# Kernel optimization log

Hardware: AMD Instinct MI355X
Metric: run time of the kernel (lower is better)

## Reference

```python
import jax, jax.numpy as jnp
import numpy as np

VOCAB, EMBED, HIDDEN, LAYERS = 128, 512, 1024, 2
BATCH, SEQ = 64, 512


def _lstm_layer(x, w_ih, w_hh, b_ih, b_hh):
    # x: [B, T, In]; w_ih: [4H, In]; w_hh: [4H, H]
    B, T, _ = x.shape
    H = w_hh.shape[1]
    # Precompute the input contribution for all timesteps at once: [B, T, 4H]
    xin = jnp.einsum('bti,gi->btg', x, w_ih) + b_ih + b_hh

    def step(carry, xt):
        h, c = carry
        z = xt + h @ w_hh.T                      # [B, 4H]
        i, f, g, o = jnp.split(z, 4, axis=-1)    # PyTorch gate order i,f,g,o
        i = jax.nn.sigmoid(i)
        f = jax.nn.sigmoid(f)
        g = jnp.tanh(g)
        o = jax.nn.sigmoid(o)
        c = f * c + i * g
        h = o * jnp.tanh(c)
        return (h, c), h

    h0 = jnp.zeros((B, H), x.dtype)
    c0 = jnp.zeros((B, H), x.dtype)
    _, hs = jax.lax.scan(step, (h0, c0), jnp.swapaxes(xin, 0, 1))  # [T, B, H]
    return jnp.swapaxes(hs, 0, 1)                                   # [B, T, H]


def setup_inputs() -> dict:
    key = jax.random.key(0)
    ks = jax.random.split(key, 12)
    s_e = 1.0 / np.sqrt(EMBED)
    s_h = 1.0 / np.sqrt(HIDDEN)
    return {
        'x': jax.random.randint(ks[0], (BATCH, SEQ), 0, VOCAB, dtype=jnp.int32),
        'embedding': jax.random.normal(ks[1], (VOCAB, EMBED), jnp.float32),
        'w_ih_0': jax.random.normal(ks[2], (4 * HIDDEN, EMBED), jnp.float32) * s_e,
        'w_hh_0': jax.random.normal(ks[3], (4 * HIDDEN, HIDDEN), jnp.float32) * s_h,
        'b_ih_0': jax.random.normal(ks[4], (4 * HIDDEN,), jnp.float32) * s_h,
        'b_hh_0': jax.random.normal(ks[5], (4 * HIDDEN,), jnp.float32) * s_h,
        'w_ih_1': jax.random.normal(ks[6], (4 * HIDDEN, HIDDEN), jnp.float32) * s_h,
        'w_hh_1': jax.random.normal(ks[7], (4 * HIDDEN, HIDDEN), jnp.float32) * s_h,
        'b_ih_1': jax.random.normal(ks[8], (4 * HIDDEN,), jnp.float32) * s_h,
        'b_hh_1': jax.random.normal(ks[9], (4 * HIDDEN,), jnp.float32) * s_h,
        'fc_w': jax.random.normal(ks[10], (VOCAB, HIDDEN), jnp.float32) * s_h,
        'fc_b': jax.random.normal(ks[11], (VOCAB,), jnp.float32) * s_h,
    }


def reference(x, embedding, w_ih_0, w_hh_0, b_ih_0, b_hh_0,
              w_ih_1, w_hh_1, b_ih_1, b_hh_1, fc_w, fc_b):
    emb = embedding[x]                                   # [B, T, E]
    h1 = _lstm_layer(emb, w_ih_0, w_hh_0, b_ih_0, b_hh_0)  # [B, T, H]
    h2 = _lstm_layer(h1, w_ih_1, w_hh_1, b_ih_1, b_hh_1)   # [B, T, H]
    return h2 @ fc_w.T + fc_b                            # [B, T, V]
```

## Files before the change

### kernel.cpp

```cpp
#include <hip/hip_runtime.h>


typedef _Float16 v8h __attribute__((ext_vector_type(8)));
typedef float v4f __attribute__((ext_vector_type(4)));
typedef _Float16 h2v __attribute__((ext_vector_type(2)));
typedef unsigned long long u64t;

__device__ __forceinline__ float sigf(float x) {
  return 1.0f / (1.0f + __expf(-x));
}
__device__ __forceinline__ float tanhfast(float x) {
  return 1.0f - 2.0f / (1.0f + __expf(2.0f * x));
}

__global__ __launch_bounds__(256) void prep_kernel(
    const float* __restrict__ emb, const float* __restrict__ w_ih0,
    const float* __restrict__ b_ih0, const float* __restrict__ b_hh0,
    const float* __restrict__ fc_w, _Float16* __restrict__ tableV,
    _Float16* __restrict__ fcwT, unsigned* __restrict__ zbuf,
    unsigned* __restrict__ bar) {
  const int blk = blockIdx.x, tid = threadIdx.x;
  if (blk < 2048) {
    const int C = blk * 2 + (tid >> 7);
    const int v = tid & 127;
    const int row =
        ((C >> 2) & 3) * 1024 + (C >> 5) * 8 + ((C >> 4) & 1) * 4 + (C & 3);
    float acc = b_ih0[row] + b_hh0[row];
    const float* er = emb + v * 512;
    const float* wr = w_ih0 + row * 512;
#pragma unroll 4
    for (int k = 0; k < 512; ++k) acc = fmaf(er[k], wr[k], acc);
    tableV[v * 4096 + C] = (_Float16)acc;
  } else if (blk < 2560) {
    const int idx = (blk - 2048) * 256 + tid;
    const int v = idx & 127, k = idx >> 7;
    fcwT[k * 128 + v] = (_Float16)fc_w[v * 1024 + k];
  } else if (blk < 2592) {
    const int idx = (blk - 2560) * 256 + tid;
#pragma unroll
    for (int q = 0; q < 16; ++q) zbuf[idx * 16 + q] = 0u;
  } else {
    for (int i = tid; i < 512; i += 256) bar[i] = 0u;
  }
}

__global__ __launch_bounds__(768, 1) void lstm_mfma(
    const int* __restrict__ x, const _Float16* __restrict__ tableV,
    const float* __restrict__ w_hh0, const float* __restrict__ w_ih1,
    const float* __restrict__ w_hh1, const float* __restrict__ b_ih1,
    const float* __restrict__ b_hh1, _Float16* __restrict__ hseq,
    unsigned* __restrict__ bar) {
  __shared__ __align__(16) float zs[12 * 4 * 8 * 32];

  const int tid = threadIdx.x, blk = blockIdx.x;
  const int w = tid >> 6, l = tid & 63;
  const int lane16 = l & 15, quad = l >> 4;
  const int xcd = blk & 7, bidx = blk >> 3;
  const int m = bidx >> 4, cg = xcd * 16 + (bidx & 15);
  const int kc = (w < 4) ? w : (w - 4);

  v8h breg0[8], breg1[8];
  {
    const int g = lane16 >> 2, j = lane16 & 3;
    const float* Wsrc;
    int kbase;
    if (w < 4) {
      Wsrc = w_hh0;
      kbase = kc * 256;
    } else {
      const int kcomb = kc * 256;
      if (kcomb < 1024) {
        Wsrc = w_ih1;
        kbase = kcomb;
      } else {
        Wsrc = w_hh1;
        kbase = kcomb - 1024;
      }
    }
#pragma unroll
    for (int cb = 0; cb < 2; ++cb) {
      const int row = g * 1024 + cg * 8 + cb * 4 + j;
      const float* rp = Wsrc + row * 1024 + kbase + quad * 8;
#pragma unroll
      for (int kk = 0; kk < 8; ++kk) {
        const float4 f0 = *(const float4*)(rp + kk * 32);
        const float4 f1 = *(const float4*)(rp + kk * 32 + 4);
        v8h b;
        b[0] = (_Float16)f0.x; b[1] = (_Float16)f0.y;
        b[2] = (_Float16)f0.z; b[3] = (_Float16)f0.w;
        b[4] = (_Float16)f1.x; b[5] = (_Float16)f1.y;
        b[6] = (_Float16)f1.z; b[7] = (_Float16)f1.w;
        if (cb == 0) breg0[kk] = b; else breg1[kk] = b;
      }
    }
  }

  const int oj = l & 7, ojj = l & 3, ocb = (l >> 2) & 1;
  const int ob = (w & 3) * 8 + (l >> 3);
  const int obg = m * 32 + ob;
  const int colp = (lane16 & 3) * 4 + (lane16 >> 2);
  const int cswz = colp ^ ((quad & 1) << 4);
  const int rr = ob & 3, rqo = ob >> 2;
  const int rcol = (ocb * 16 + ojj * 4) ^ ((rqo & 1) << 4);

  v4f bias4 = {0.f, 0.f, 0.f, 0.f};
  if (w >= 4 && w < 8) {
#pragma unroll
    for (int g = 0; g < 4; ++g) {
      const int row = g * 1024 + cg * 8 + ocb * 4 + ojj;
      bias4[g] = b_ih1[row] + b_hh1[row];
    }
  }
  _Float16 tvh[4] = {0, 0, 0, 0};
  if (w < 4) {
    const int xv = x[obg * 512];
#pragma unroll
    for (int g = 0; g < 4; ++g)
      tvh[g] = tableV[xv * 4096 + cg * 32 + ocb * 16 + g * 4 + ojj];
  }

  float cst = 0.0f;
  const int gq = blk & 7;

  for (int it = 0; it <= 512; ++it) {
    const _Float16* hr = hseq + (size_t)it * 131072;
    _Float16* hw = hseq + (size_t)(it + 1) * 131072;

    v4f a00 = {0, 0, 0, 0}, a01 = {0, 0, 0, 0};
    v4f a10 = {0, 0, 0, 0}, a11 = {0, 0, 0, 0};
    const bool active = (w < 4) ? (it < 512) : (it >= 1);
    if (active) {
      const _Float16* a0p = hr + (m * 32 + lane16) * 2048 + kc * 256 + quad * 8;
      const _Float16* a1p = a0p + 16 * 2048;
      v8h A0[8], A1[8];
#pragma unroll
      for (int kk = 0; kk < 8; ++kk) A0[kk] = *(const v8h*)(a0p + kk * 32);
#pragma unroll
      for (int kk = 0; kk < 8; ++kk) A1[kk] = *(const v8h*)(a1p + kk * 32);
      __builtin_amdgcn_sched_barrier(0);
#pragma unroll
      for (int kk = 0; kk < 8; ++kk) {
        a00 = __builtin_amdgcn_mfma_f32_16x16x32_f16(A0[kk], breg0[kk], a00, 0, 0, 0);
        a10 = __builtin_amdgcn_mfma_f32_16x16x32_f16(A0[kk], breg1[kk], a10, 0, 0, 0);
      }
#pragma unroll
      for (int kk = 0; kk < 8; ++kk) {
        a01 = __builtin_amdgcn_mfma_f32_16x16x32_f16(A1[kk], breg0[kk], a01, 0, 0, 0);
        a11 = __builtin_amdgcn_mfma_f32_16x16x32_f16(A1[kk], breg1[kk], a11, 0, 0, 0);
      }
    }

#pragma unroll
    for (int r = 0; r < 4; ++r) {
      float* zp = &zs[((w * 4 + r) * 8 + quad) * 32];
      zp[cswz] = a00[r];
      zp[128 + cswz] = a01[r];
      zp[cswz ^ 16] = a10[r];
      zp[128 + (cswz ^ 16)] = a11[r];
    }
    __syncthreads();

    const bool do0 = (w < 4) && (it < 512);
    const bool do1 = (w >= 4 && w < 8) && (it >= 1);
    if (do0 || do1) {
      v4f z;
      if (do0) {
        z[0] = (float)tvh[0]; z[1] = (float)tvh[1];
        z[2] = (float)tvh[2]; z[3] = (float)tvh[3];
#pragma unroll
        for (int wv = 0; wv < 4; ++wv)
          z += *(const v4f*)&zs[((wv * 4 + rr) * 8 + rqo) * 32 + rcol];
      } else {
        z = bias4;
#pragma unroll
        for (int wv = 4; wv < 12; ++wv)
          z += *(const v4f*)&zs[((wv * 4 + rr) * 8 + rqo) * 32 + rcol];
      }
      const float ig = sigf(z[0]), fg = sigf(z[1]);
      const float gg = tanhfast(z[2]), og = sigf(z[3]);
      cst = fg * cst + ig * gg;
      const float hv = og * tanhfast(cst);

      const unsigned hu =
          (unsigned)__builtin_bit_cast(unsigned short, (_Float16)hv);
      const unsigned p1 = (unsigned)__shfl_xor((int)hu, 1, 64);
      const unsigned lo = (oj & 1) ? ((p1 & 0xffffu) | (hu << 16))
                                   : ((hu & 0xffffu) | (p1 << 16));
      const unsigned p2 = (unsigned)__shfl_xor((int)lo, 2, 64);
      if ((oj & 3) == 0) {
        const u64t val = (u64t)lo | ((u64t)p2 << 32);
        if (do0) {
          __hip_atomic_store((u64t*)(hw + obg * 2048 + cg * 8 + oj), val,
                             __ATOMIC_RELAXED, __HIP_MEMORY_SCOPE_AGENT);
        } else {
          __hip_atomic_store((u64t*)(hw + obg * 2048 + 1024 + cg * 8 + oj),
                             val, __ATOMIC_RELAXED, __HIP_MEMORY_SCOPE_AGENT);
        }
      }
    }

    if (w < 4 && it + 1 < 512) {
      const int xv = x[obg * 512 + it + 1];
#pragma unroll
      for (int g = 0; g < 4; ++g)
        tvh[g] = tableV[xv * 4096 + cg * 32 + ocb * 16 + g * 4 + ojj];
    }

    if (it < 512) {
      asm volatile("s_waitcnt vmcnt(0)" ::: "memory");
      __syncthreads();
      if (tid == 0) {
        atomicAdd(&bar[(m * 8 + gq) * 16], 1u);
        const unsigned tgt = 16u * (unsigned)(it + 1);
        for (;;) {
          unsigned v[8];
#pragma unroll
          for (int g = 0; g < 8; ++g)
            v[g] = __hip_atomic_load(&bar[(m * 8 + g) * 16], __ATOMIC_RELAXED,
                                     __HIP_MEMORY_SCOPE_AGENT);
          unsigned mn = v[0];
#pragma unroll
          for (int g = 1; g < 8; ++g) mn = (v[g] < mn) ? v[g] : mn;
          if (mn >= tgt) break;
          __builtin_amdgcn_s_sleep(1);
        }
      }
      __syncthreads();
      asm volatile("" ::: "memory");
    }
  }
}

__global__ __launch_bounds__(256, 2) void fc_kernel(
    const _Float16* __restrict__ hseq, const _Float16* __restrict__ fcwT,
    const float* __restrict__ fc_b, float* __restrict__ out) {
  __shared__ float hl[16][1024];
  const int tid = threadIdx.x;
  const int t = blockIdx.x >> 2, bs = blockIdx.x & 3;
  const int v = tid & 127, hh = tid >> 7;

  const h2v* hp = (const h2v*)hseq;
  const size_t base = (size_t)(t + 2) * 65536 + 512;
  for (int idx = tid; idx < 8192; idx += 256) {
    const int bl = idx >> 9, kp = idx & 511;
    const h2v pr = hp[base + (size_t)((bs * 16 + bl)) * 1024 + kp];
    hl[bl][2 * kp] = (float)pr.x;
    hl[bl][2 * kp + 1] = (float)pr.y;
  }
  __syncthreads();

  float acc[8];
#pragma unroll
  for (int i = 0; i < 8; ++i) acc[i] = 0.0f;
  const int bl0 = hh * 8;
#pragma unroll 1
  for (int k4 = 0; k4 < 256; ++k4) {
    const int k = k4 * 4;
    const float w0 = (float)fcwT[(k + 0) * 128 + v];
    const float w1 = (float)fcwT[(k + 1) * 128 + v];
    const float w2 = (float)fcwT[(k + 2) * 128 + v];
    const float w3 = (float)fcwT[(k + 3) * 128 + v];
#pragma unroll
    for (int i = 0; i < 8; ++i) {
      const float4 hv = *(const float4*)&hl[bl0 + i][k];
      acc[i] += hv.x * w0 + hv.y * w1 + hv.z * w2 + hv.w * w3;
    }
  }
  const float bias = fc_b[v];
#pragma unroll
  for (int i = 0; i < 8; ++i) {
    const int bb = bs * 16 + bl0 + i;
    out[(bb * 512 + t) * 128 + v] = acc[i] + bias;
  }
}

extern "C" void kernel_launch(void* const* d_in, const int* in_sizes, int n_in,
                              void* d_out, int out_size, void* d_ws,
                              size_t ws_size, hipStream_t stream) {
  const int* x = (const int*)d_in[0];
  const float* emb = (const float*)d_in[1];
  const float* w_ih0 = (const float*)d_in[2];
  const float* w_hh0 = (const float*)d_in[3];
  const float* b_ih0 = (const float*)d_in[4];
  const float* b_hh0 = (const float*)d_in[5];
  const float* w_ih1 = (const float*)d_in[6];
  const float* w_hh1 = (const float*)d_in[7];
  const float* b_ih1 = (const float*)d_in[8];
  const float* b_hh1 = (const float*)d_in[9];
  const float* fc_w = (const float*)d_in[10];
  const float* fc_b = (const float*)d_in[11];
  float* out = (float*)d_out;

  char* ws = (char*)d_ws;
  _Float16* tableV = (_Float16*)(ws);
  _Float16* fcwT = (_Float16*)(ws + 1048576);
  unsigned* bar = (unsigned*)(ws + 1310720);
  _Float16* hseq = (_Float16*)(ws + 1376256);
  unsigned* zb = (unsigned*)(ws + 1376256);

  prep_kernel<<<2593, 256, 0, stream>>>(emb, w_ih0, b_ih0, b_hh0, fc_w,
                                        tableV, fcwT, zb, bar);

  const _Float16* tableVc = tableV;
  _Float16* hseqa = hseq;
  unsigned* bara = bar;
  void* args[] = {(void*)&x,     (void*)&tableVc, (void*)&w_hh0,
                  (void*)&w_ih1, (void*)&w_hh1,   (void*)&b_ih1,
                  (void*)&b_hh1, (void*)&hseqa,   (void*)&bara};
  hipLaunchCooperativeKernel(lstm_mfma, dim3(256), dim3(768), args, 0, stream);

  fc_kernel<<<2048, 256, 0, stream>>>(hseq, fcwT, fc_b, out);
}
```

Measured before the change: 4.878 ms.

## Reuse layer-0 h tile for both w_hh0 and w_ih1 products, shrink block to 8 waves

Warps 0-3 now hold both the w_hh0 and w_ih1 weight slices in registers and apply both to the same loaded h1 tile, so the layer-1 input projection no longer needs separate waves that reload the same h data. The block shrinks from 12 to 8 waves, and launch bounds change to 512 threads with 2 blocks per CU. This removes redundant global loads of h and frees waves, but it doubles the B-register footprint in waves 0-3, which increases register pressure and risks spills. It also puts more serial MFMA work on those waves.

```diff
diff --git a/kernel.cpp b/kernel.cpp
--- a/kernel.cpp
+++ b/kernel.cpp
@@ -44,7 +44,7 @@
   }
 }
 
-__global__ __launch_bounds__(768, 1) void lstm_mfma(
+__global__ __launch_bounds__(512, 2) void lstm_mfma(
     const int* __restrict__ x, const _Float16* __restrict__ tableV,
     const float* __restrict__ w_hh0, const float* __restrict__ w_ih1,
     const float* __restrict__ w_hh1, const float* __restrict__ b_ih1,
@@ -57,26 +57,12 @@
   const int lane16 = l & 15, quad = l >> 4;
   const int xcd = blk & 7, bidx = blk >> 3;
   const int m = bidx >> 4, cg = xcd * 16 + (bidx & 15);
-  const int kc = (w < 4) ? w : (w - 4);
-
-  v8h breg0[8], breg1[8];
+
+  v8h bh0[8], bh1[8], bi0[8], bi1[8];
   {
     const int g = lane16 >> 2, j = lane16 & 3;
-    const float* Wsrc;
-    int kbase;
-    if (w < 4) {
-      Wsrc = w_hh0;
-      kbase = kc * 256;
-    } else {
-      const int kcomb = kc * 256;
-      if (kcomb < 1024) {
-        Wsrc = w_ih1;
-        kbase = kcomb;
-      } else {
-        Wsrc = w_hh1;
-        kbase = kcomb - 1024;
-      }
-    }
+    const float* Wsrc = (w < 4) ? w_hh0 : w_hh1;
+    const int kbase = (w < 4) ? w * 256 : w * 256 - 1024;
 #pragma unroll
     for (int cb = 0; cb < 2; ++cb) {
       const int row = g * 1024 + cg * 8 + cb * 4 + j;
@@ -90,7 +76,25 @@
         b[2] = (_Float16)f0.z; b[3] = (_Float16)f0.w;
         b[4] = (_Float16)f1.x; b[5] = (_Float16)f1.y;
         b[6] = (_Float16)f1.z; b[7] = (_Float16)f1.w;
-        if (cb == 0) breg0[kk] = b; else breg1[kk] = b;
+        if (cb == 0) bh0[kk] = b; else bh1[kk] = b;
+      }
+    }
+    if (w < 4) {
+#pragma unroll
+      for (int cb = 0; cb < 2; ++cb) {
+        const int row = g * 1024 + cg * 8 + cb * 4 + j;
+        const float* rp = w_ih1 + row * 1024 + w * 256 + quad * 8;
+#pragma unroll
+        for (int kk = 0; kk < 8; ++kk) {
+          const float4 f0 = *(const float4*)(rp + kk * 32);
+          const float4 f1 = *(const float4*)(rp + kk * 32 + 4);
+          v8h b;
+          b[0] = (_Float16)f0.x; b[1] = (_Float16)f0.y;
+          b[2] = (_Float16)f0.z; b[3] = (_Float16)f0.w;
+          b[4] = (_Float16)f1.x; b[5] = (_Float16)f1.y;
+          b[6] = (_Float16)f1.z; b[7] = (_Float16)f1.w;
+          if (cb == 0) bi0[kk] = b; else bi1[kk] = b;
+        }
       }
     }
   }
@@ -104,7 +108,7 @@
   const int rcol = (ocb * 16 + ojj * 4) ^ ((rqo & 1) << 4);
 
   v4f bias4 = {0.f, 0.f, 0.f, 0.f};
-  if (w >= 4 && w < 8) {
+  if (w >= 4) {
 #pragma unroll
     for (int g = 0; g < 4; ++g) {
       const int row = g * 1024 + cg * 8 + ocb * 4 + ojj;
@@ -126,11 +130,13 @@
     const _Float16* hr = hseq + (size_t)it * 131072;
     _Float16* hw = hseq + (size_t)(it + 1) * 131072;
 
-    v4f a00 = {0, 0, 0, 0}, a01 = {0, 0, 0, 0};
-    v4f a10 = {0, 0, 0, 0}, a11 = {0, 0, 0, 0};
-    const bool active = (w < 4) ? (it < 512) : (it >= 1);
-    if (active) {
-      const _Float16* a0p = hr + (m * 32 + lane16) * 2048 + kc * 256 + quad * 8;
+    v4f p00 = {0, 0, 0, 0}, p01 = {0, 0, 0, 0};
+    v4f p10 = {0, 0, 0, 0}, p11 = {0, 0, 0, 0};
+    v4f q00 = {0, 0, 0, 0}, q01 = {0, 0, 0, 0};
+    v4f q10 = {0, 0, 0, 0}, q11 = {0, 0, 0, 0};
+    const bool ld = (w < 4) || (it >= 1);
+    if (ld) {
+      const _Float16* a0p = hr + (m * 32 + lane16) * 2048 + w * 256 + quad * 8;
       const _Float16* a1p = a0p + 16 * 2048;
       v8h A0[8], A1[8];
 #pragma unroll
@@ -138,30 +144,64 @@
 #pragma unroll
       for (int kk = 0; kk < 8; ++kk) A1[kk] = *(const v8h*)(a1p + kk * 32);
       __builtin_amdgcn_sched_barrier(0);
-#pragma unroll
-      for (int kk = 0; kk < 8; ++kk) {
-        a00 = __builtin_amdgcn_mfma_f32_16x16x32_f16(A0[kk], breg0[kk], a00, 0, 0, 0);
-        a10 = __builtin_amdgcn_mfma_f32_16x16x32_f16(A0[kk], breg1[kk], a10, 0, 0, 0);
-      }
-#pragma unroll
-      for (int kk = 0; kk < 8; ++kk) {
-        a01 = __builtin_amdgcn_mfma_f32_16x16x32_f16(A1[kk], breg0[kk], a01, 0, 0, 0);
-        a11 = __builtin_amdgcn_mfma_f32_16x16x32_f16(A1[kk], breg1[kk], a11, 0, 0, 0);
-      }
-    }
-
-#pragma unroll
-    for (int r = 0; r < 4; ++r) {
-      float* zp = &zs[((w * 4 + r) * 8 + quad) * 32];
-      zp[cswz] = a00[r];
-      zp[128 + cswz] = a01[r];
-      zp[cswz ^ 16] = a10[r];
-      zp[128 + (cswz ^ 16)] = a11[r];
+      if (w < 4) {
+        if (it < 512) {
+#pragma unroll
+          for (int kk = 0; kk < 8; ++kk) {
+            p00 = __builtin_amdgcn_mfma_f32_16x16x32_f16(A0[kk], bh0[kk], p00, 0, 0, 0);
+            p10 = __builtin_amdgcn_mfma_f32_16x16x32_f16(A0[kk], bh1[kk], p10, 0, 0, 0);
+            p01 = __builtin_amdgcn_mfma_f32_16x16x32_f16(A1[kk], bh0[kk], p01, 0, 0, 0);
+            p11 = __builtin_amdgcn_mfma_f32_16x16x32_f16(A1[kk], bh1[kk], p11, 0, 0, 0);
+          }
+        }
+        if (it >= 1) {
+#pragma unroll
+          for (int kk = 0; kk < 8; ++kk) {
+            q00 = __builtin_amdgcn_mfma_f32_16x16x32_f16(A0[kk], bi0[kk], q00, 0, 0, 0);
+            q10 = __builtin_amdgcn_mfma_f32_16x16x32_f16(A0[kk], bi1[kk], q10, 0, 0, 0);
+            q01 = __builtin_amdgcn_mfma_f32_16x16x32_f16(A1[kk], bi0[kk], q01, 0, 0, 0);
+            q11 = __builtin_amdgcn_mfma_f32_16x16x32_f16(A1[kk], bi1[kk], q11, 0, 0, 0);
+          }
+        }
+      } else {
+#pragma unroll
+        for (int kk = 0; kk < 8; ++kk) {
+          p00 = __builtin_amdgcn_mfma_f32_16x16x32_f16(A0[kk], bh0[kk], p00, 0, 0, 0);
+          p10 = __builtin_amdgcn_mfma_f32_16x16x32_f16(A0[kk], bh1[kk], p10, 0, 0, 0);
+          p01 = __builtin_amdgcn_mfma_f32_16x16x32_f16(A1[kk], bh0[kk], p01, 0, 0, 0);
+          p11 = __builtin_amdgcn_mfma_f32_16x16x32_f16(A1[kk], bh1[kk], p11, 0, 0, 0);
+        }
+      }
+    }
+
+    if (w < 4) {
+#pragma unroll
+      for (int r = 0; r < 4; ++r) {
+        float* zpa = &zs[((w * 4 + r) * 8 + quad) * 32];
+        zpa[cswz] = p00[r];
+        zpa[128 + cswz] = p01[r];
+        zpa[cswz ^ 16] = p10[r];
+        zpa[128 + (cswz ^ 16)] = p11[r];
+        float* zpb = &zs[(((w + 4) * 4 + r) * 8 + quad) * 32];
+        zpb[cswz] = q00[r];
+        zpb[128 + cswz] = q01[r];
+        zpb[cswz ^ 16] = q10[r];
+        zpb[128 + (cswz ^ 16)] = q11[r];
+      }
+    } else {
+#pragma unroll
+      for (int r = 0; r < 4; ++r) {
+        float* zpb = &zs[(((w + 4) * 4 + r) * 8 + quad) * 32];
+        zpb[cswz] = p00[r];
+        zpb[128 + cswz] = p01[r];
+        zpb[cswz ^ 16] = p10[r];
+        zpb[128 + (cswz ^ 16)] = p11[r];
+      }
     }
     __syncthreads();
 
     const bool do0 = (w < 4) && (it < 512);
-    const bool do1 = (w >= 4 && w < 8) && (it >= 1);
+    const bool do1 = (w >= 4) && (it >= 1);
     if (do0 || do1) {
       v4f z;
       if (do0) {
@@ -307,7 +347,7 @@
   void* args[] = {(void*)&x,     (void*)&tableVc, (void*)&w_hh0,
                   (void*)&w_ih1, (void*)&w_hh1,   (void*)&b_ih1,
                   (void*)&b_hh1, (void*)&hseqa,   (void*)&bara};
-  hipLaunchCooperativeKernel(lstm_mfma, dim3(256), dim3(768), args, 0, stream);
+  hipLaunchCooperativeKernel(lstm_mfma, dim3(256), dim3(512), args, 0, stream);
 
   fc_kernel<<<2048, 256, 0, stream>>>(hseq, fcwT, fc_b, out);
 }
```

Measured after the change: 4.244 ms. 1.15x faster.
